# Optimization experiments

Hardware: AMD Instinct MI355X
Metric: run time of the kernel (lower is better)

## Reference

```python
import jax, jax.numpy as jnp
import numpy as np

B, I, DI, O, DO = 256, 1152, 8, 10, 16
ROUTING_ITERS = 3


def squash(s):
    # squash along last dim (out_capsule_dim); keepdims version of the
    # module's intended math: v = s * |s|^2 / (1+|s|^2) / |s|
    sq = jnp.sum(s * s, axis=-1, keepdims=True)
    return s * sq / (1.0 + sq) / jnp.sqrt(sq)


def setup_inputs() -> dict:
    key = jax.random.key(0)
    k1, k2 = jax.random.split(key)
    x = jax.random.normal(k1, (B, I, DI), dtype=jnp.float32)
    stdv = 1.0 / np.sqrt(I)
    W = jax.random.uniform(k2, (I, O, DO, DI), dtype=jnp.float32,
                           minval=-stdv, maxval=stdv)
    return {"x": x, "W": W}


def reference(x, W):
    # u_hat[b,i,o,d] = W[i,o,d,k] @ x[b,i,k]
    u_hat = jnp.einsum('iodk,bik->biod', W, x)  # [B, I, O, DO]
    u_det = jax.lax.stop_gradient(u_hat)
    b_ij = jnp.zeros((B, I, O), dtype=u_hat.dtype)
    v = None
    for it in range(ROUTING_ITERS):
        c = jax.nn.softmax(b_ij, axis=2)              # softmax over out caps
        uh = u_hat if it == ROUTING_ITERS - 1 else u_det
        s = jnp.einsum('bio,biod->bod', c, uh)        # [B, O, DO]
        v = squash(s)
        if it < ROUTING_ITERS - 1:
            b_ij = b_ij + jnp.einsum('biod,bod->bio', u_det, v)
    return v  # [B, O, DO]
```

## Files before the change

### kernel.cpp

```cpp
#include <hip/hip_runtime.h>
#include <hip/hip_fp16.h>
#include <math.h>


constexpr int Bc  = 256;
constexpr int Ic  = 1152;
constexpr int Oc  = 10;
constexpr int DOc = 16;
constexpr int ODc = 160;

__global__ __launch_bounds__(256, 4) void k_uhat(const float* __restrict__ x,
                                                 const float* __restrict__ W,
                                                 __half2* __restrict__ uws,
                                                 float* __restrict__ partial) {
    const int bx    = blockIdx.x;
    const int itile = bx % 72;
    const int btile = bx / 72;
    const int t     = threadIdx.x;
    const int d     = t & 15;
    const int il    = t >> 4;
    const int w     = t >> 6;
    const int i     = itile * 16 + il;
    const int b0    = btile * 16;

    __shared__ __align__(16) float xs[16 * 128];
    __shared__ __align__(16) float pacc[4 * 16 * ODc];

#pragma unroll
    for (int j = 0; j < 2; ++j) {
        int e  = t + j * 256;
        int bb = e >> 5;
        int r  = e & 31;
        ((float4*)xs)[e] =
            ((const float4*)(x + (size_t)(b0 + bb) * (Ic * 8) + itile * 128))[r];
    }

    float4 wr[20];
    {
        const float4* wp = (const float4*)(W + (((size_t)i * Oc) * DOc + d) * 8);
#pragma unroll
        for (int o = 0; o < Oc; ++o) {
            wr[2 * o]     = wp[o * 32];
            wr[2 * o + 1] = wp[o * 32 + 1];
        }
    }
    __syncthreads();

    const int ch    = i >> 6;
    const int off_t = (i & 63) * 16 + d;

#pragma unroll 1
    for (int bb = 0; bb < 16; ++bb) {
        const int b = b0 + bb;
        const float4 xa = *((const float4*)(xs + bb * 128 + il * 8));
        const float4 xb = *((const float4*)(xs + bb * 128 + il * 8 + 4));
        float u[Oc];
#pragma unroll
        for (int o = 0; o < Oc; ++o) {
            float4 w0 = wr[2 * o], w1 = wr[2 * o + 1];
            u[o] = w0.x * xa.x + w0.y * xa.y + w0.z * xa.z + w0.w * xa.w +
                   w1.x * xb.x + w1.y * xb.y + w1.z * xb.z + w1.w * xb.w;
        }
        __half2* ub = uws + ((size_t)b * 90 + ch * 5) * 1024 + off_t;
#pragma unroll
        for (int op = 0; op < 5; ++op)
            ub[op * 1024] = __floats2half2_rn(u[2 * op], u[2 * op + 1]);
#pragma unroll
        for (int o = 0; o < Oc; ++o) {
            float a = u[o];
            a += __shfl_xor(a, 16);
            a += __shfl_xor(a, 32);
            if ((t & 63) < 16) pacc[(w * 16 + bb) * ODc + o * 16 + d] = a;
        }
    }
    __syncthreads();
#pragma unroll
    for (int j = 0; j < 10; ++j) {
        int e = t + j * 256;
        float s = pacc[e] + pacc[2560 + e] + pacc[5120 + e] + pacc[7680 + e];
        partial[(size_t)itile * (Bc * ODc) + b0 * ODc + e] = s;
    }
}

template <int P, int MODE>
__global__ __launch_bounds__(256) void k_squash(const float* __restrict__ part,
                                                float* __restrict__ vsum,
                                                float* __restrict__ out,
                                                float pre) {
    const int b = blockIdx.x;
    const int t = threadIdx.x;
    if (t >= ODc) return;
    float s = 0.f;
#pragma unroll 8
    for (int p = 0; p < P; ++p) s += part[(size_t)p * (Bc * ODc) + b * ODc + t];
    s *= pre;
    float sq = s * s;
    sq += __shfl_xor(sq, 1);
    sq += __shfl_xor(sq, 2);
    sq += __shfl_xor(sq, 4);
    sq += __shfl_xor(sq, 8);
    float scale = sq / ((1.f + sq) * sqrtf(sq));
    float v = s * scale;
    if (MODE == 0) vsum[b * ODc + t] = v;
    if (MODE == 1) vsum[b * ODc + t] += v;
    if (MODE == 2) out[b * ODc + t] = v;
}

__global__ __launch_bounds__(1024, 8) void k_route(const __half2* __restrict__ uws,
                                                   const float* __restrict__ vsum,
                                                   float* __restrict__ spart) {
    const int bx  = blockIdx.x;
    const int b   = bx >> 1;
    const int h   = bx & 1;
    const int t   = threadIdx.x;
    const int d   = t & 15;
    const int wid = t >> 6;

    __shared__ float vs_s[ODc];
    __shared__ float red[16 * ODc];
    if (t < ODc) vs_s[t] = vsum[b * ODc + t];
    __syncthreads();

    float vsr[Oc];
#pragma unroll
    for (int o = 0; o < Oc; ++o) vsr[o] = vs_s[o * 16 + d];
    float acc[Oc];
#pragma unroll
    for (int o = 0; o < Oc; ++o) acc[o] = 0.f;

    const __half2* wsb = uws + ((size_t)b * 90 + h * 45) * 1024 + t;
#pragma unroll 1
    for (int ch = 0; ch < 9; ++ch) {
        float uo[Oc];
#pragma unroll
        for (int op = 0; op < 5; ++op) {
            float2 f = __half22float2(wsb[(ch * 5 + op) * 1024]);
            uo[2 * op]     = f.x;
            uo[2 * op + 1] = f.y;
        }
        float c[Oc];
#pragma unroll
        for (int o = 0; o < Oc; ++o) {
            float p = uo[o] * vsr[o];
            p += __shfl_xor(p, 1);
            p += __shfl_xor(p, 2);
            p += __shfl_xor(p, 4);
            p += __shfl_xor(p, 8);
            c[o] = p;
        }
        float m = c[0];
#pragma unroll
        for (int o = 1; o < Oc; ++o) m = fmaxf(m, c[o]);
        float se = 0.f;
#pragma unroll
        for (int o = 0; o < Oc; ++o) {
            c[o] = __expf(c[o] - m);
            se += c[o];
        }
        const float inv = 1.f / se;
#pragma unroll
        for (int o = 0; o < Oc; ++o) acc[o] += (c[o] * inv) * uo[o];
    }
#pragma unroll
    for (int o = 0; o < Oc; ++o) {
        float a = acc[o];
        a += __shfl_xor(a, 16);
        a += __shfl_xor(a, 32);
        if ((t & 63) < 16) red[wid * ODc + o * 16 + (t & 15)] = a;
    }
    __syncthreads();
    if (t < ODc) {
        float s = 0.f;
#pragma unroll
        for (int w = 0; w < 16; ++w) s += red[w * ODc + t];
        spart[(size_t)h * (Bc * ODc) + b * ODc + t] = s;
    }
}

__global__ void __launch_bounds__(1024, 4)
digitcaps_fallback(const float* __restrict__ x, const float* __restrict__ W,
                   float* __restrict__ out) {
    const int b = blockIdx.x, t = threadIdx.x;
    const int lane = t & 63, wid = t >> 6, d = t & 15, iblk = t >> 4;
    __shared__ __align__(16) float xs[Ic * 8];
    __shared__ __align__(16) float red[16 * ODc];
    __shared__ __align__(16) float svec[ODc], vcur[ODc], vsum[ODc];
    {
        const float4* xg = (const float4*)(x + (size_t)b * (Ic * 8));
        float4* xl = (float4*)xs;
        for (int j = t; j < Ic * 2; j += 1024) xl[j] = xg[j];
    }
    if (t < ODc) vsum[t] = 0.f;
    __syncthreads();
    float acc[Oc], vsr[Oc];
    for (int it = 0; it < 3; ++it) {
#pragma unroll
        for (int o = 0; o < Oc; ++o) { acc[o] = 0.f; vsr[o] = vsum[o * 16 + d]; }
#pragma unroll 1
        for (int chk = 0; chk < 18; ++chk) {
            const int i = chk * 64 + iblk;
            const float4 xa = ((const float4*)(xs + i * 8))[0];
            const float4 xb = ((const float4*)(xs + i * 8))[1];
            const float* wb = W + (((size_t)i * Oc) * DOc + d) * 8;
            float uo[Oc];
#pragma unroll
            for (int o = 0; o < Oc; ++o) {
                const float4* wp = (const float4*)(wb + o * 128);
                float4 w0 = wp[0], w1 = wp[1];
                uo[o] = w0.x * xa.x + w0.y * xa.y + w0.z * xa.z + w0.w * xa.w +
                        w1.x * xb.x + w1.y * xb.y + w1.z * xb.z + w1.w * xb.w;
            }
            float cc[Oc];
            if (it > 0) {
#pragma unroll
                for (int o = 0; o < Oc; ++o) {
                    float p = uo[o] * vsr[o];
                    p += __shfl_xor(p, 1); p += __shfl_xor(p, 2);
                    p += __shfl_xor(p, 4); p += __shfl_xor(p, 8);
                    cc[o] = p;
                }
                float m = cc[0];
#pragma unroll
                for (int o = 1; o < Oc; ++o) m = fmaxf(m, cc[o]);
                float se = 0.f;
#pragma unroll
                for (int o = 0; o < Oc; ++o) { cc[o] = __expf(cc[o] - m); se += cc[o]; }
                float inv = 1.f / se;
#pragma unroll
                for (int o = 0; o < Oc; ++o) acc[o] += cc[o] * inv * uo[o];
            } else {
#pragma unroll
                for (int o = 0; o < Oc; ++o) acc[o] += 0.1f * uo[o];
            }
        }
#pragma unroll
        for (int o = 0; o < Oc; ++o) {
            float a = acc[o];
            a += __shfl_xor(a, 16);
            a += __shfl_xor(a, 32);
            if (lane < 16) red[wid * ODc + o * 16 + lane] = a;
        }
        __syncthreads();
        if (t < ODc) {
            float s = 0.f;
#pragma unroll
            for (int w = 0; w < 16; ++w) s += red[w * ODc + t];
            svec[t] = s;
        }
        __syncthreads();
        if (t < Oc) {
            float sq = 0.f;
#pragma unroll
            for (int dd = 0; dd < DOc; ++dd) sq += svec[t * 16 + dd] * svec[t * 16 + dd];
            float sc = sq / ((1.f + sq) * sqrtf(sq));
#pragma unroll
            for (int dd = 0; dd < DOc; ++dd) {
                float v = svec[t * 16 + dd] * sc;
                vcur[t * 16 + dd] = v;
                vsum[t * 16 + dd] += v;
            }
        }
        __syncthreads();
    }
    if (t < ODc) out[(size_t)b * ODc + t] = vcur[t];
}

extern "C" void kernel_launch(void* const* d_in, const int* in_sizes, int n_in,
                              void* d_out, int out_size, void* d_ws, size_t ws_size,
                              hipStream_t stream) {
    (void)in_sizes; (void)n_in; (void)out_size;
    const float* x = (const float*)d_in[0];
    const float* W = (const float*)d_in[1];
    float* out     = (float*)d_out;

    const size_t UWS_B  = (size_t)Bc * 90 * 1024 * sizeof(__half2);
    const size_t PART_B = (size_t)72 * Bc * ODc * sizeof(float);
    const size_t SPART_B = (size_t)2 * Bc * ODc * sizeof(float);
    const size_t VSUM_B  = (size_t)Bc * ODc * sizeof(float);

    __half2* uws   = (__half2*)d_ws;
    float* partial = (float*)((char*)d_ws + UWS_B);
    float* spart   = (float*)((char*)d_ws + UWS_B + PART_B);
    float* vsum    = (float*)((char*)d_ws + UWS_B + PART_B + SPART_B);

    if (ws_size >= UWS_B + PART_B + SPART_B + VSUM_B) {
        hipLaunchKernelGGL(k_uhat, dim3(1152), dim3(256), 0, stream, x, W, uws, partial);
        hipLaunchKernelGGL((k_squash<72, 0>), dim3(Bc), dim3(256), 0, stream,
                           partial, vsum, out, 0.1f);
        hipLaunchKernelGGL(k_route, dim3(512), dim3(1024), 0, stream, uws, vsum, spart);
        hipLaunchKernelGGL((k_squash<2, 1>), dim3(Bc), dim3(256), 0, stream,
                           spart, vsum, out, 1.f);
        hipLaunchKernelGGL(k_route, dim3(512), dim3(1024), 0, stream, uws, vsum, spart);
        hipLaunchKernelGGL((k_squash<2, 2>), dim3(Bc), dim3(256), 0, stream,
                           spart, vsum, out, 1.f);
    } else {
        hipLaunchKernelGGL(digitcaps_fallback, dim3(Bc), dim3(1024), 0, stream,
                           x, W, out);
    }
}
```

Before: 182.0 us.

## Recompute u_hat in each routing pass instead of storing fp16 workspace

Removes the fp16 u_hat workspace (about 94MB of writes and two re-reads). Every routing pass now recomputes u_hat from x and W inside a templated k_pass kernel, with the softmax routing fused in. Cross-lane 16-wide reductions switch from shuffles to DPP row operations. The trade is recomputing the matmul three times, plus two extra 72-way partial reductions in squash where there were 2-way ones.

New measurement: 267.1 us. 46.8% more time.

```diff
diff --git a/kernel.cpp b/kernel.cpp
--- a/kernel.cpp
+++ b/kernel.cpp
@@ -1,5 +1,4 @@
 #include <hip/hip_runtime.h>
-#include <hip/hip_fp16.h>
 #include <math.h>
 
 
@@ -8,14 +7,29 @@
 constexpr int Oc  = 10;
 constexpr int DOc = 16;
 constexpr int ODc = 160;
-
-__global__ __launch_bounds__(256, 4) void k_uhat(const float* __restrict__ x,
+constexpr int ITILES = 72;
+
+__device__ __forceinline__ float dpp16_sum(float v) {
+    int s;
+    s = __builtin_amdgcn_update_dpp(0, __float_as_int(v), 0xB1, 0xF, 0xF, true);
+    v += __int_as_float(s);
+    s = __builtin_amdgcn_update_dpp(0, __float_as_int(v), 0x4E, 0xF, 0xF, true);
+    v += __int_as_float(s);
+    s = __builtin_amdgcn_update_dpp(0, __float_as_int(v), 0x124, 0xF, 0xF, true);
+    v += __int_as_float(s);
+    s = __builtin_amdgcn_update_dpp(0, __float_as_int(v), 0x128, 0xF, 0xF, true);
+    v += __int_as_float(s);
+    return v;
+}
+
+template <int PASS>
+__global__ __launch_bounds__(256, 2) void k_pass(const float* __restrict__ x,
                                                  const float* __restrict__ W,
-                                                 __half2* __restrict__ uws,
+                                                 const float* __restrict__ vsum,
                                                  float* __restrict__ partial) {
     const int bx    = blockIdx.x;
-    const int itile = bx % 72;
-    const int btile = bx / 72;
+    const int itile = bx % ITILES;
+    const int btile = bx / ITILES;
     const int t     = threadIdx.x;
     const int d     = t & 15;
     const int il    = t >> 4;
@@ -25,6 +39,7 @@
 
     __shared__ __align__(16) float xs[16 * 128];
     __shared__ __align__(16) float pacc[4 * 16 * ODc];
+    __shared__ __align__(16) float vs_s[16 * ODc];
 
 #pragma unroll
     for (int j = 0; j < 2; ++j) {
@@ -34,6 +49,14 @@
         ((float4*)xs)[e] =
             ((const float4*)(x + (size_t)(b0 + bb) * (Ic * 8) + itile * 128))[r];
     }
+    if (PASS == 1) {
+        const float4* vg = (const float4*)(vsum + (size_t)b0 * ODc);
+#pragma unroll
+        for (int j = 0; j < 3; ++j) {
+            int e = t + j * 256;
+            if (e < 640) ((float4*)vs_s)[e] = vg[e];
+        }
+    }
 
     float4 wr[20];
     {
@@ -46,12 +69,8 @@
     }
     __syncthreads();
 
-    const int ch    = i >> 6;
-    const int off_t = (i & 63) * 16 + d;
-
 #pragma unroll 1
     for (int bb = 0; bb < 16; ++bb) {
-        const int b = b0 + bb;
         const float4 xa = *((const float4*)(xs + bb * 128 + il * 8));
         const float4 xb = *((const float4*)(xs + bb * 128 + il * 8 + 4));
         float u[Oc];
@@ -61,13 +80,31 @@
             u[o] = w0.x * xa.x + w0.y * xa.y + w0.z * xa.z + w0.w * xa.w +
                    w1.x * xb.x + w1.y * xb.y + w1.z * xb.z + w1.w * xb.w;
         }
-        __half2* ub = uws + ((size_t)b * 90 + ch * 5) * 1024 + off_t;
-#pragma unroll
-        for (int op = 0; op < 5; ++op)
-            ub[op * 1024] = __floats2half2_rn(u[2 * op], u[2 * op + 1]);
-#pragma unroll
-        for (int o = 0; o < Oc; ++o) {
-            float a = u[o];
+        float contrib[Oc];
+        if (PASS == 1) {
+            float c[Oc];
+#pragma unroll
+            for (int o = 0; o < Oc; ++o)
+                c[o] = dpp16_sum(u[o] * vs_s[bb * ODc + o * 16 + d]);
+            float m = c[0];
+#pragma unroll
+            for (int o = 1; o < Oc; ++o) m = fmaxf(m, c[o]);
+            float se = 0.f;
+#pragma unroll
+            for (int o = 0; o < Oc; ++o) {
+                c[o] = __expf(c[o] - m);
+                se += c[o];
+            }
+            const float inv = 1.f / se;
+#pragma unroll
+            for (int o = 0; o < Oc; ++o) contrib[o] = (c[o] * inv) * u[o];
+        } else {
+#pragma unroll
+            for (int o = 0; o < Oc; ++o) contrib[o] = u[o];
+        }
+#pragma unroll
+        for (int o = 0; o < Oc; ++o) {
+            float a = contrib[o];
             a += __shfl_xor(a, 16);
             a += __shfl_xor(a, 32);
             if ((t & 63) < 16) pacc[(w * 16 + bb) * ODc + o * 16 + d] = a;
@@ -82,7 +119,7 @@
     }
 }
 
-template <int P, int MODE>
+template <int MODE>
 __global__ __launch_bounds__(256) void k_squash(const float* __restrict__ part,
                                                 float* __restrict__ vsum,
                                                 float* __restrict__ out,
@@ -92,89 +129,15 @@
     if (t >= ODc) return;
     float s = 0.f;
 #pragma unroll 8
-    for (int p = 0; p < P; ++p) s += part[(size_t)p * (Bc * ODc) + b * ODc + t];
+    for (int p = 0; p < ITILES; ++p)
+        s += part[(size_t)p * (Bc * ODc) + b * ODc + t];
     s *= pre;
-    float sq = s * s;
-    sq += __shfl_xor(sq, 1);
-    sq += __shfl_xor(sq, 2);
-    sq += __shfl_xor(sq, 4);
-    sq += __shfl_xor(sq, 8);
+    float sq = dpp16_sum(s * s);
     float scale = sq / ((1.f + sq) * sqrtf(sq));
     float v = s * scale;
     if (MODE == 0) vsum[b * ODc + t] = v;
     if (MODE == 1) vsum[b * ODc + t] += v;
-    if (MODE == 2) out[b * ODc + t] = v;
-}
-
-__global__ __launch_bounds__(1024, 8) void k_route(const __half2* __restrict__ uws,
-                                                   const float* __restrict__ vsum,
-                                                   float* __restrict__ spart) {
-    const int bx  = blockIdx.x;
-    const int b   = bx >> 1;
-    const int h   = bx & 1;
-    const int t   = threadIdx.x;
-    const int d   = t & 15;
-    const int wid = t >> 6;
-
-    __shared__ float vs_s[ODc];
-    __shared__ float red[16 * ODc];
-    if (t < ODc) vs_s[t] = vsum[b * ODc + t];
-    __syncthreads();
-
-    float vsr[Oc];
-#pragma unroll
-    for (int o = 0; o < Oc; ++o) vsr[o] = vs_s[o * 16 + d];
-    float acc[Oc];
-#pragma unroll
-    for (int o = 0; o < Oc; ++o) acc[o] = 0.f;
-
-    const __half2* wsb = uws + ((size_t)b * 90 + h * 45) * 1024 + t;
-#pragma unroll 1
-    for (int ch = 0; ch < 9; ++ch) {
-        float uo[Oc];
-#pragma unroll
-        for (int op = 0; op < 5; ++op) {
-            float2 f = __half22float2(wsb[(ch * 5 + op) * 1024]);
-            uo[2 * op]     = f.x;
-            uo[2 * op + 1] = f.y;
-        }
-        float c[Oc];
-#pragma unroll
-        for (int o = 0; o < Oc; ++o) {
-            float p = uo[o] * vsr[o];
-            p += __shfl_xor(p, 1);
-            p += __shfl_xor(p, 2);
-            p += __shfl_xor(p, 4);
-            p += __shfl_xor(p, 8);
-            c[o] = p;
-        }
-        float m = c[0];
-#pragma unroll
-        for (int o = 1; o < Oc; ++o) m = fmaxf(m, c[o]);
-        float se = 0.f;
-#pragma unroll
-        for (int o = 0; o < Oc; ++o) {
-            c[o] = __expf(c[o] - m);
-            se += c[o];
-        }
-        const float inv = 1.f / se;
-#pragma unroll
-        for (int o = 0; o < Oc; ++o) acc[o] += (c[o] * inv) * uo[o];
-    }
-#pragma unroll
-    for (int o = 0; o < Oc; ++o) {
-        float a = acc[o];
-        a += __shfl_xor(a, 16);
-        a += __shfl_xor(a, 32);
-        if ((t & 63) < 16) red[wid * ODc + o * 16 + (t & 15)] = a;
-    }
-    __syncthreads();
-    if (t < ODc) {
-        float s = 0.f;
-#pragma unroll
-        for (int w = 0; w < 16; ++w) s += red[w * ODc + t];
-        spart[(size_t)h * (Bc * ODc) + b * ODc + t] = s;
-    }
+    if (MODE == 2) out[(size_t)b * ODc + t] = v;
 }
 
 __global__ void __launch_bounds__(1024, 4)
@@ -213,12 +176,7 @@
             float cc[Oc];
             if (it > 0) {
 #pragma unroll
-                for (int o = 0; o < Oc; ++o) {
-                    float p = uo[o] * vsr[o];
-                    p += __shfl_xor(p, 1); p += __shfl_xor(p, 2);
-                    p += __shfl_xor(p, 4); p += __shfl_xor(p, 8);
-                    cc[o] = p;
-                }
+                for (int o = 0; o < Oc; ++o) cc[o] = dpp16_sum(uo[o] * vsr[o]);
                 float m = cc[0];
 #pragma unroll
                 for (int o = 1; o < Oc; ++o) m = fmaxf(m, cc[o]);
@@ -273,26 +231,23 @@
     const float* W = (const float*)d_in[1];
     float* out     = (float*)d_out;
 
-    const size_t UWS_B  = (size_t)Bc * 90 * 1024 * sizeof(__half2);
-    const size_t PART_B = (size_t)72 * Bc * ODc * sizeof(float);
-    const size_t SPART_B = (size_t)2 * Bc * ODc * sizeof(float);
-    const size_t VSUM_B  = (size_t)Bc * ODc * sizeof(float);
-
-    __half2* uws   = (__half2*)d_ws;
-    float* partial = (float*)((char*)d_ws + UWS_B);
-    float* spart   = (float*)((char*)d_ws + UWS_B + PART_B);
-    float* vsum    = (float*)((char*)d_ws + UWS_B + PART_B + SPART_B);
-
-    if (ws_size >= UWS_B + PART_B + SPART_B + VSUM_B) {
-        hipLaunchKernelGGL(k_uhat, dim3(1152), dim3(256), 0, stream, x, W, uws, partial);
-        hipLaunchKernelGGL((k_squash<72, 0>), dim3(Bc), dim3(256), 0, stream,
+    const size_t PART_B = (size_t)ITILES * Bc * ODc * sizeof(float);
+    const size_t VSUM_B = (size_t)Bc * ODc * sizeof(float);
+
+    float* partial = (float*)d_ws;
+    float* vsum    = (float*)((char*)d_ws + PART_B);
+
+    if (ws_size >= PART_B + VSUM_B) {
+        dim3 pg(ITILES * 16), pb(256);
+        hipLaunchKernelGGL((k_pass<0>), pg, pb, 0, stream, x, W, nullptr, partial);
+        hipLaunchKernelGGL((k_squash<0>), dim3(Bc), dim3(256), 0, stream,
                            partial, vsum, out, 0.1f);
-        hipLaunchKernelGGL(k_route, dim3(512), dim3(1024), 0, stream, uws, vsum, spart);
-        hipLaunchKernelGGL((k_squash<2, 1>), dim3(Bc), dim3(256), 0, stream,
-                           spart, vsum, out, 1.f);
-        hipLaunchKernelGGL(k_route, dim3(512), dim3(1024), 0, stream, uws, vsum, spart);
-        hipLaunchKernelGGL((k_squash<2, 2>), dim3(Bc), dim3(256), 0, stream,
-                           spart, vsum, out, 1.f);
+        hipLaunchKernelGGL((k_pass<1>), pg, pb, 0, stream, x, W, vsum, partial);
+        hipLaunchKernelGGL((k_squash<1>), dim3(Bc), dim3(256), 0, stream,
+                           partial, vsum, out, 1.f);
+        hipLaunchKernelGGL((k_pass<1>), pg, pb, 0, stream, x, W, vsum, partial);
+        hipLaunchKernelGGL((k_squash<2>), dim3(Bc), dim3(256), 0, stream,
+                           partial, vsum, out, 1.f);
     } else {
         hipLaunchKernelGGL(digitcaps_fallback, dim3(Bc), dim3(1024), 0, stream,
                            x, W, out);
```
